# Kernel tuning notes

Measured on AMD Instinct MI355X. Metric: run time of the kernel, lower is better.

Reference implementation:

```python
import jax, jax.numpy as jnp
import numpy as np

P = 7            # cfg.PATCH_SIZE_PHOTOMETRIC
BRIGHT = 0.02    # bright_threshold
BIG = 1e9        # masks invalid points out of kNN
K = 5            # neighbors for smoothness/slope


def _smooth_l1(x, y, beta):
    d = jnp.abs(x - y)
    return jnp.where(d < beta, 0.5 * d * d / beta, d - 0.5 * beta)


def _sample_patches(img, kp):
    # img: [B,1,H,W], kp: [B,N,2] (x,y) in pixel coords -> [B,1,N,P,P]
    # matches F.grid_sample(align_corners=True, bilinear, border): with the
    # module's normalization, sampling positions are exactly pixel coords.
    B, _, H, W = img.shape
    N = kp.shape[1]
    half = P // 2
    lin = jnp.linspace(-half, half, P)
    oy, ox = jnp.meshgrid(lin, lin, indexing='ij')  # patch index (i,j): +x=lin[j], +y=lin[i]
    px = jnp.clip(kp[..., 0:1] + ox.ravel(), 0.0, W - 1)  # [B,N,P*P]
    py = jnp.clip(kp[..., 1:2] + oy.ravel(), 0.0, H - 1)
    x0 = jnp.floor(px); y0 = jnp.floor(py)
    fx = px - x0; fy = py - y0
    x0i = jnp.clip(x0.astype(jnp.int32), 0, W - 1)
    x1i = jnp.clip(x0i + 1, 0, W - 1)
    y0i = jnp.clip(y0.astype(jnp.int32), 0, H - 1)
    y1i = jnp.clip(y0i + 1, 0, H - 1)
    im = img[:, 0]  # [B,H,W]
    b = jnp.arange(B)[:, None, None]
    v00 = im[b, y0i, x0i]; v01 = im[b, y0i, x1i]
    v10 = im[b, y1i, x0i]; v11 = im[b, y1i, x1i]
    val = (v00 * (1 - fx) + v01 * fx) * (1 - fy) + (v10 * (1 - fx) + v11 * fx) * fy
    return val.reshape(B, 1, N, P, P)


def _forward(lg, rg, kpl, kpr, scores, Q):
    B, N, _ = kpl.shape
    # ---- epipolar ----
    y_diff = jnp.abs(kpl[..., 1] - kpr[..., 1])
    ws = scores.sum()
    l_epipolar = jnp.where(ws > 1e-4, (y_diff * scores).sum() / jnp.maximum(ws, 1e-12), y_diff.mean())
    # ---- photometric + intensity ----
    pl = _sample_patches(lg, kpl)
    pr = _sample_patches(rg, kpr)
    c = P // 2
    center_l = pl[:, 0, :, c, c]  # [B,N]
    center_r = pr[:, 0, :, c, c]
    is_bright = (center_l > BRIGHT).astype(pl.dtype)
    diff = jnp.abs(pl - pr).mean(axis=(1, 3, 4))  # [B,N]
    w = scores * is_bright
    wsum = w.sum()
    safe = jnp.maximum(wsum, 1e-12)
    l_masked = jnp.where(wsum > 1e-4, (diff * w).sum() / safe, 0.0)
    l_intensity = jnp.where(wsum > 1e-4, (_smooth_l1(center_l, center_r, 1.0) * w).sum() / safe, 0.0)
    l_photo = l_masked + l_intensity
    # ---- disparity -> 3D ----
    disp = kpl[..., 0] - kpr[..., 0]
    pts4 = jnp.concatenate([kpl, disp[..., None], jnp.ones((B, N, 1), kpl.dtype)], axis=-1)
    proj = jnp.einsum('bni,bji->bnj', pts4, Q)
    Wc = jnp.maximum(proj[..., 3], 1e-6)
    p3d = proj[..., :3] / Wc[..., None]  # [B,N,3]
    Z = p3d[..., 2]
    valid = (Z > 100) & (Z < 30000) & (scores > 0.1)  # [B,N]
    # ---- kNN smoothness / slope / zero-mean (masked, vectorized) ----
    pm = p3d / 1000.0
    xy = pm[..., jnp.array([0, 2])]  # [B,N,2] horizontal plane
    h = pm[..., 1]                   # [B,N] height
    sq = (xy * xy).sum(-1)
    d2 = sq[:, :, None] + sq[:, None, :] - 2.0 * jnp.einsum('bnd,bmd->bnm', xy, xy)
    dist = jnp.sqrt(jnp.maximum(d2, 1e-12))  # [B,N,N]
    vm = valid[:, :, None] & valid[:, None, :]
    dist = jnp.where(vm, dist, BIG)
    negd, idx = jax.lax.top_k(-dist, K + 1)   # ascending distance
    nbr_idx = idx[:, :, 1:]                   # drop self
    nbr_d = jnp.maximum(-negd[:, :, 1:], 1e-3)
    b = jnp.arange(B)[:, None, None]
    nbr_h = h[b, nbr_idx]                     # [B,N,K]
    local_mean = nbr_h.mean(-1)
    n_valid = valid.sum(-1)
    nv = jnp.maximum(n_valid, 1).astype(h.dtype)
    vf = valid.astype(h.dtype)
    ls_b = (_smooth_l1(h, local_mean, 0.01) * vf).sum(-1) / nv
    slopes = jnp.abs(nbr_h - h[..., None]) / nbr_d
    pen = jax.nn.relu(slopes - 0.4)
    lsl_b = (pen * vf[..., None]).sum((-1, -2)) / (nv * K)
    lz_b = jnp.abs((h * vf).sum(-1) / nv)
    ok = (n_valid >= 10).astype(h.dtype)
    nb = jnp.maximum(ok.sum(), 1.0)
    gate = ((scores > 0.1).sum() >= 10) & (ok.sum() > 0)
    l_smooth = jnp.where(gate, (ls_b * ok).sum() / nb, 0.0)
    l_slope = jnp.where(gate, (lsl_b * ok).sum() / nb, 0.0)
    l_zeromean = jnp.where(gate, (lz_b * ok).sum() / nb, 0.0)
    return (l_photo, l_epipolar, l_smooth, l_slope, l_zeromean)


def setup_inputs() -> dict:
    key = jax.random.key(0)
    k = jax.random.split(key, 7)
    B, N, H, W = 16, 2000, 720, 1280
    lg = jax.random.uniform(k[0], (B, 1, H, W), dtype=jnp.float32)
    rg = jax.random.uniform(k[1], (B, 1, H, W), dtype=jnp.float32)
    kx = jax.random.uniform(k[2], (B, N), minval=200.0, maxval=1080.0)
    ky = jax.random.uniform(k[3], (B, N), minval=50.0, maxval=670.0)
    disp = jax.random.uniform(k[4], (B, N), minval=10.0, maxval=200.0)
    kpl = jnp.stack([kx, ky], -1)
    kpr = jnp.stack([kx - disp, ky + 0.5 * jax.random.normal(k[5], (B, N))], -1)
    scores = jax.random.uniform(k[6], (B, N), dtype=jnp.float32)
    f, cx, cy, Tx = 1000.0, 640.0, 360.0, 120.0  # focal px, principal point, baseline mm
    Qm = jnp.array([[1.0, 0.0, 0.0, -cx],
                    [0.0, 1.0, 0.0, -cy],
                    [0.0, 0.0, 0.0, f],
                    [0.0, 0.0, 1.0 / Tx, 0.0]], dtype=jnp.float32)
    Q = jnp.broadcast_to(Qm, (B, 4, 4))
    return {"lg": lg, "rg": rg, "kpl": kpl, "kpr": kpr, "scores": scores, "Q": Q}


def reference(lg, rg, kpl, kpr, scores, Q):
    return _forward(lg, rg, kpl, kpr, scores, Q)
```

## Files before the change

### kernel.cpp

```cpp
#include <hip/hip_runtime.h>

#define BB 16
#define NN 2000
#define HH 720
#define WW 1280
#define NPT (BB*NN)
#define PATCH_BLOCKS (NPT/32)
#define PROJ_BLOCKS (NPT/256)
#define KSTRIDE 2048
#define MAX_SEG 500

static __device__ __forceinline__ unsigned u_min(unsigned a, unsigned b){ return a < b ? a : b; }

static __device__ __forceinline__ unsigned u_med3(unsigned a, unsigned b, unsigned c) {
    unsigned d;
    asm("v_med3_u32 %0, %1, %2, %3" : "=v"(d) : "v"(a), "v"(b), "v"(c));
    return d;
}

__device__ __forceinline__ void ins5(unsigned K[5], unsigned u) {
    K[4] = u_med3(K[3], K[4], u);
    K[3] = u_med3(K[2], K[3], u);
    K[2] = u_med3(K[1], K[2], u);
    K[1] = u_med3(K[0], K[1], u);
    K[0] = u_min(K[0], u);
}

__device__ __forceinline__ float bilin(const float* __restrict__ im, float px, float py) {
    px = fminf(fmaxf(px, 0.f), (float)(WW - 1));
    py = fminf(fmaxf(py, 0.f), (float)(HH - 1));
    float x0f = floorf(px), y0f = floorf(py);
    float fx = px - x0f, fy = py - y0f;
    int x0 = min(max((int)x0f, 0), WW - 1);
    int x1 = min(x0 + 1, WW - 1);
    int y0 = min(max((int)y0f, 0), HH - 1);
    int y1 = min(y0 + 1, HH - 1);
    const float* r0 = im + (size_t)y0 * WW;
    const float* r1 = im + (size_t)y1 * WW;
    float v00 = r0[x0], v01 = r0[x1], v10 = r1[x0], v11 = r1[x1];
    return (v00 * (1.f - fx) + v01 * fx) * (1.f - fy)
         + (v10 * (1.f - fx) + v11 * fx) * fy;
}

__global__ __launch_bounds__(256) void project_kernel(
    const float* __restrict__ kpl, const float* __restrict__ kpr,
    const float* __restrict__ scores, const float* __restrict__ Q,
    float4* __restrict__ pts, float* __restrict__ partialsA,
    float* __restrict__ batch_acc, unsigned* __restrict__ dcnt)
{
    if (blockIdx.x == 0) {
        if (threadIdx.x < BB * 4) batch_acc[threadIdx.x] = 0.f;
        if (threadIdx.x == BB * 4) *dcnt = 0u;
    }
    int pt = blockIdx.x * 256 + threadIdx.x;
    int b  = pt / NN;

    float2 kl = ((const float2* __restrict__)kpl)[pt];
    float2 kr = ((const float2* __restrict__)kpr)[pt];
    float sc  = scores[pt];
    float ydiff = fabsf(kl.y - kr.y);

    const float* q = Q + b * 16;
    float dsp = kl.x - kr.x;
    float p0 = q[0]*kl.x  + q[1]*kl.y  + q[2]*dsp  + q[3];
    float p1 = q[4]*kl.x  + q[5]*kl.y  + q[6]*dsp  + q[7];
    float p2 = q[8]*kl.x  + q[9]*kl.y  + q[10]*dsp + q[11];
    float p3 = q[12]*kl.x + q[13]*kl.y + q[14]*dsp + q[15];
    float Wc = fmaxf(p3, 1e-6f);
    float X = p0 / Wc, Y = p1 / Wc, Z = p2 / Wc;
    bool valid = (Z > 100.f) && (Z < 30000.f) && (sc > 0.1f);
    float x  = X / 1000.f;
    float hh = Y / 1000.f;
    float y  = Z / 1000.f;
    float sq = x * x + y * y;
    if (!valid) { x = 0.f; y = 0.f; sq = 1e18f; }
    pts[pt] = make_float4(x, y, sq, hh);

    float s0 = sc, s1 = ydiff * sc, s2 = ydiff, s3 = (sc > 0.1f) ? 1.f : 0.f;
    #pragma unroll
    for (int off = 32; off > 0; off >>= 1) {
        s0 += __shfl_down(s0, off, 64);
        s1 += __shfl_down(s1, off, 64);
        s2 += __shfl_down(s2, off, 64);
        s3 += __shfl_down(s3, off, 64);
    }
    __shared__ float red[4][4];
    int wave = threadIdx.x >> 6, lane = threadIdx.x & 63;
    if (lane == 0) { red[wave][0]=s0; red[wave][1]=s1; red[wave][2]=s2; red[wave][3]=s3; }
    __syncthreads();
    if (threadIdx.x < 4) {
        int k = threadIdx.x;
        partialsA[blockIdx.x * 4 + k] = red[0][k] + red[1][k] + red[2][k] + red[3][k];
    }
}

__global__ __launch_bounds__(256) void fused_patch_scan(
    const float* __restrict__ lg, const float* __restrict__ rg,
    const float* __restrict__ kpl, const float* __restrict__ kpr,
    const float* __restrict__ scores,
    const float4* __restrict__ pts, unsigned* __restrict__ keybuf,
    float* __restrict__ partialsB, int msegLen, int lns, int interleave)
{
    int i = blockIdx.x;
    int pid, sid;
    if (interleave) {
        if ((i % 3 == 1) && (i < 3000)) { pid = i / 3;  sid = -1; }
        else { pid = -1; sid = i - ((i < 3000) ? (i + 2) / 3 : 1000); }
    } else {
        if (i < PATCH_BLOCKS) { pid = i; sid = -1; }
        else { pid = -1; sid = i - PATCH_BLOCKS; }
    }

    if (pid >= 0) {
        int wave = threadIdx.x >> 6, lane = threadIdx.x & 63;
        int rr = lane / 7, ci = lane - rr * 7;
        int s00 = lane + rr;
        if (s00 > 54) s00 = 54;
        int reg_r = lane >> 3, reg_c = lane & 7;

        float a3 = 0.f, a4l = 0.f, a5 = 0.f;

        for (int it = 0; it < 8; ++it) {
            int pt = pid * 32 + wave * 8 + it;
            int b = pt / NN;
            const float* iml = lg + (size_t)b * (HH * WW);
            const float* imr = rg + (size_t)b * (HH * WW);
            float kxl = kpl[2*pt], kyl = kpl[2*pt+1];
            float kxr = kpr[2*pt], kyr = kpr[2*pt+1];
            float sc  = scores[pt];

            float flx = floorf(kxl), fly = floorf(kyl);
            int xbl = (int)flx - 3, ybl = (int)fly - 3;
            float fxl = kxl - flx, fyl = kyl - fly;
            float vl = 0.f;
            if (xbl >= 0 && xbl <= WW-8 && ybl >= 0 && ybl <= HH-8) {
                float reg = iml[(size_t)(ybl + reg_r) * WW + xbl + reg_c];
                float v00 = __shfl(reg, s00,     64);
                float v01 = __shfl(reg, s00 + 1, 64);
                float v10 = __shfl(reg, s00 + 8, 64);
                float v11 = __shfl(reg, s00 + 9, 64);
                vl = (v00*(1.f-fxl) + v01*fxl)*(1.f-fyl) + (v10*(1.f-fxl) + v11*fxl)*fyl;
            } else if (lane < 49) {
                vl = bilin(iml, kxl + (float)(ci-3), kyl + (float)(rr-3));
            }
            float frx = floorf(kxr), fry = floorf(kyr);
            int xbr = (int)frx - 3, ybr = (int)fry - 3;
            float fxr = kxr - frx, fyr = kyr - fry;
            float vr = 0.f;
            if (xbr >= 0 && xbr <= WW-8 && ybr >= 0 && ybr <= HH-8) {
                float reg = imr[(size_t)(ybr + reg_r) * WW + xbr + reg_c];
                float v00 = __shfl(reg, s00,     64);
                float v01 = __shfl(reg, s00 + 1, 64);
                float v10 = __shfl(reg, s00 + 8, 64);
                float v11 = __shfl(reg, s00 + 9, 64);
                vr = (v00*(1.f-fxr) + v01*fxr)*(1.f-fyr) + (v10*(1.f-fxr) + v11*fxr)*fyr;
            } else if (lane < 49) {
                vr = bilin(imr, kxr + (float)(ci-3), kyr + (float)(rr-3));
            }

            float adiff = (lane < 49) ? fabsf(vl - vr) : 0.f;
            float cl = __shfl(vl, 24, 64);
            float cr = __shfl(vr, 24, 64);

            float isb = (cl > 0.02f) ? 1.f : 0.f;
            float w   = sc * isb;
            float dc  = fabsf(cl - cr);
            float sl1 = (dc < 1.f) ? 0.5f * dc * dc : dc - 0.5f;

            a3 += w;
            a5 += sl1 * w;
            a4l += w * adiff;
        }

        #pragma unroll
        for (int off = 32; off > 0; off >>= 1) a4l += __shfl_down(a4l, off, 64);

        __shared__ float red[4][3];
        if (lane == 0) { red[wave][0]=a3; red[wave][1]=a4l * (1.f/49.f); red[wave][2]=a5; }
        __syncthreads();
        if (threadIdx.x < 4) {
            int k = threadIdx.x;
            float v = 0.f;
            if (k < 3) v = red[0][k] + red[1][k] + red[2][k] + red[3][k];
            partialsB[pid * 4 + k] = v;
        }
    } else {
        __shared__ float4 seg[MAX_SEG];
        int sblk = sid;
        int bx   = sblk & 7;
        int r    = sblk >> 3;
        int segi = r & ((1 << lns) - 1);
        int b    = r >> lns;
        int ns   = 1 << lns;
        int mseg0 = segi * msegLen;
        int n = bx * 256 + threadIdx.x;
        int nc = (n < NN) ? n : (NN - 1);

        const float4* cand = pts + b * NN + mseg0;
        for (int j = threadIdx.x; j < msegLen; j += 256) seg[j] = cand[j];

        float4 me = pts[b * NN + nc];
        float nx2 = -2.f * me.x, ny2 = -2.f * me.y, sqn = me.z;

        unsigned K[5] = {0xFFFFFFFFu,0xFFFFFFFFu,0xFFFFFFFFu,0xFFFFFFFFu,0xFFFFFFFFu};

        int nb0 = bx * 256;
        bool has_self = (mseg0 < nb0 + 256) && (mseg0 + msegLen > nb0);

        __syncthreads();

        if (has_self) {
            #pragma unroll 5
            for (int mm = 0; mm < msegLen; ++mm) {
                float4 o = seg[mm];
                int m = mseg0 + mm;
                float t = fmaf(ny2, o.y, o.z);
                t = fmaf(nx2, o.x, t);
                float d2 = fmaxf(t + sqn, 1e-12f);
                unsigned u = (__float_as_uint(d2) & 0xFFFFF800u) | (unsigned)m;
                u = (m == n) ? 0xFFFFFFFFu : u;
                ins5(K, u);
            }
        } else {
            #pragma unroll 5
            for (int mm = 0; mm < msegLen; ++mm) {
                float4 o = seg[mm];
                int m = mseg0 + mm;
                float t = fmaf(ny2, o.y, o.z);
                t = fmaf(nx2, o.x, t);
                float d2 = fmaxf(t + sqn, 1e-12f);
                unsigned u = (__float_as_uint(d2) & 0xFFFFF800u) | (unsigned)m;
                ins5(K, u);
            }
        }

        if (n < NN) {
            size_t base = (size_t)((b * ns + segi) * 5) * KSTRIDE + n;
            keybuf[base              ] = K[0];
            keybuf[base + KSTRIDE    ] = K[1];
            keybuf[base + KSTRIDE * 2] = K[2];
            keybuf[base + KSTRIDE * 3] = K[3];
            keybuf[base + KSTRIDE * 4] = K[4];
        }
    }
}

__global__ __launch_bounds__(256) void knn_merge_final(
    const float4* __restrict__ pts, const unsigned* __restrict__ keybuf,
    float* __restrict__ batch_acc, unsigned* __restrict__ dcnt,
    const float* __restrict__ partialsA, const float* __restrict__ partialsB,
    float* __restrict__ out, int ns)
{
    int b = blockIdx.y;
    int n = blockIdx.x * 256 + threadIdx.x;

    float ls = 0.f, pen = 0.f, hacc = 0.f, cnt = 0.f;
    if (n < NN) {
        float4 me = pts[b * NN + n];
        if (me.z < 1e17f) {
            unsigned K[5] = {0xFFFFFFFFu,0xFFFFFFFFu,0xFFFFFFFFu,0xFFFFFFFFu,0xFFFFFFFFu};
            for (int s = 0; s < ns; ++s) {
                #pragma unroll
                for (int j = 0; j < 5; ++j) {
                    unsigned u = keybuf[(size_t)((b * ns + s) * 5 + j) * KSTRIDE + n];
                    ins5(K, u);
                }
            }
            float hsum = 0.f;
            #pragma unroll
            for (int t = 0; t < 5; ++t) {
                int idx = (int)(K[t] & 2047u);
                float4 o = pts[b * NN + idx];
                float dot = me.x * o.x + me.y * o.y;
                float d2 = (me.z + o.z) - 2.f * dot;
                float nd = fmaxf(sqrtf(fmaxf(d2, 1e-12f)), 0.001f);
                hsum += o.w;
                pen  += fmaxf(fabsf(o.w - me.w) / nd - 0.4f, 0.f);
            }
            float lm = hsum / 5.f;
            float dd = fabsf(me.w - lm);
            ls = (dd < 0.01f) ? 0.5f * dd * dd / 0.01f : dd - 0.005f;
            hacc = me.w;
            cnt  = 1.f;
        }
    }

    #pragma unroll
    for (int off = 32; off > 0; off >>= 1) {
        ls   += __shfl_down(ls,   off, 64);
        pen  += __shfl_down(pen,  off, 64);
        hacc += __shfl_down(hacc, off, 64);
        cnt  += __shfl_down(cnt,  off, 64);
    }
    __shared__ float r2[4][4];
    int wave = threadIdx.x >> 6, lane = threadIdx.x & 63;
    if (lane == 0) { r2[wave][0]=cnt; r2[wave][1]=ls; r2[wave][2]=pen; r2[wave][3]=hacc; }
    __syncthreads();
    if (threadIdx.x == 0) {
        float tc = r2[0][0]+r2[1][0]+r2[2][0]+r2[3][0];
        float tl = r2[0][1]+r2[1][1]+r2[2][1]+r2[3][1];
        float tp = r2[0][2]+r2[1][2]+r2[2][2]+r2[3][2];
        float th = r2[0][3]+r2[1][3]+r2[2][3]+r2[3][3];
        atomicAdd(&batch_acc[b * 4 + 0], tc);
        atomicAdd(&batch_acc[b * 4 + 1], tl);
        atomicAdd(&batch_acc[b * 4 + 2], tp);
        atomicAdd(&batch_acc[b * 4 + 3], th);
    }

    __shared__ int lastf;
    __threadfence();
    if (threadIdx.x == 0) {
        unsigned old = atomicAdd(dcnt, 1u);
        lastf = (old == (unsigned)(8 * BB - 1)) ? 1 : 0;
    }
    __syncthreads();
    if (!lastf) return;
    __threadfence();

    float s[7] = {0,0,0,0,0,0,0};
    for (int rI = threadIdx.x; rI < PROJ_BLOCKS; rI += 256) {
        s[0] += partialsA[rI * 4 + 0];
        s[1] += partialsA[rI * 4 + 1];
        s[2] += partialsA[rI * 4 + 2];
        s[3] += partialsA[rI * 4 + 3];
    }
    for (int rI = threadIdx.x; rI < PATCH_BLOCKS; rI += 256) {
        s[4] += partialsB[rI * 4 + 0];
        s[5] += partialsB[rI * 4 + 1];
        s[6] += partialsB[rI * 4 + 2];
    }
    #pragma unroll
    for (int off = 32; off > 0; off >>= 1) {
        #pragma unroll
        for (int k = 0; k < 7; ++k) s[k] += __shfl_down(s[k], off, 64);
    }
    __shared__ float ws2[4][7];
    if (lane == 0) {
        #pragma unroll
        for (int k = 0; k < 7; ++k) ws2[wave][k] = s[k];
    }
    __syncthreads();
    if (threadIdx.x == 0) {
        float t[7];
        #pragma unroll
        for (int k = 0; k < 7; ++k)
            t[k] = ws2[0][k] + ws2[1][k] + ws2[2][k] + ws2[3][k];
        float ssc = t[0], yds = t[1], yd = t[2], cnts = t[3];
        float wsum = t[4], dw = t[5], iw = t[6];

        float l_epi = (ssc > 1e-4f) ? yds / fmaxf(ssc, 1e-12f) : yd / (float)NPT;
        float safe = fmaxf(wsum, 1e-12f);
        float l_photo = (wsum > 1e-4f) ? (dw / safe + iw / safe) : 0.f;

        float als = 0.f, alsl = 0.f, alz = 0.f, okc = 0.f;
        for (int bb = 0; bb < BB; ++bb) {
            float nvf  = __hip_atomic_load(&batch_acc[bb*4+0], __ATOMIC_RELAXED, __HIP_MEMORY_SCOPE_AGENT);
            float lsb  = __hip_atomic_load(&batch_acc[bb*4+1], __ATOMIC_RELAXED, __HIP_MEMORY_SCOPE_AGENT);
            float penb = __hip_atomic_load(&batch_acc[bb*4+2], __ATOMIC_RELAXED, __HIP_MEMORY_SCOPE_AGENT);
            float hb   = __hip_atomic_load(&batch_acc[bb*4+3], __ATOMIC_RELAXED, __HIP_MEMORY_SCOPE_AGENT);
            float nv = fmaxf(nvf, 1.f);
            float ok = (nvf >= 10.f) ? 1.f : 0.f;
            als  += ok * (lsb / nv);
            alsl += ok * (penb / (nv * 5.f));
            alz  += ok * fabsf(hb / nv);
            okc  += ok;
        }
        float nb = fmaxf(okc, 1.f);
        bool gate = (cnts >= 10.f) && (okc > 0.f);
        out[0] = l_photo;
        out[1] = l_epi;
        out[2] = gate ? als / nb : 0.f;
        out[3] = gate ? alsl / nb : 0.f;
        out[4] = gate ? alz / nb : 0.f;
    }
}

extern "C" void kernel_launch(void* const* d_in, const int* in_sizes, int n_in,
                              void* d_out, int out_size, void* d_ws, size_t ws_size,
                              hipStream_t stream)
{
    const float* lg     = (const float*)d_in[0];
    const float* rg     = (const float*)d_in[1];
    const float* kpl    = (const float*)d_in[2];
    const float* kpr    = (const float*)d_in[3];
    const float* scores = (const float*)d_in[4];
    const float* Q      = (const float*)d_in[5];
    float* out = (float*)d_out;

    char* ws = (char*)d_ws;
    float4*   pts       = (float4*)ws;
    float*    partialsA = (float*)(ws + 512000);
    float*    partialsB = (float*)(ws + 514048);
    float*    batch_acc = (float*)(ws + 530432);
    unsigned* dcnt      = (unsigned*)(ws + 530688);
    unsigned* keybuf    = (unsigned*)(ws + 530944);

    int ns = 16;
    if (ws_size < 530944 + (size_t)BB * 16 * 5 * KSTRIDE * 4) ns = 8;
    if (ws_size < 530944 + (size_t)BB *  8 * 5 * KSTRIDE * 4) ns = 4;
    int lns = (ns == 16) ? 4 : ((ns == 8) ? 3 : 2);
    int msegLen = NN / ns;
    int interleave = (ns == 16) ? 1 : 0;

    project_kernel<<<PROJ_BLOCKS, 256, 0, stream>>>(kpl, kpr, scores, Q,
                                                    pts, partialsA, batch_acc, dcnt);
    fused_patch_scan<<<PATCH_BLOCKS + 8 * ns * BB, 256, 0, stream>>>(
        lg, rg, kpl, kpr, scores, pts, keybuf, partialsB, msegLen, lns, interleave);
    knn_merge_final<<<dim3(8, BB), 256, 0, stream>>>(pts, keybuf, batch_acc, dcnt,
                                                     partialsA, partialsB, out, ns);
}
```

Measured before the change: 178.7 us.

## Split patch work to one point per wave and interleave 4:1 with scan blocks

The patch-sampling part of the fused kernel now gives each wave a single keypoint instead of looping over eight, so there are 8000 patch blocks instead of 1000. Patch blocks are interleaved four to one with kNN scan blocks, and the left and right image loads are issued together before the shuffles. The goal is more memory-level parallelism and better load balance between the two block types. The cost is more blocks, a larger partials buffer (workspace offsets shift) and a longer final reduction over 8000 partials.

```diff
diff --git a/kernel.cpp b/kernel.cpp
--- a/kernel.cpp
+++ b/kernel.cpp
@@ -5,7 +5,7 @@
 #define HH 720
 #define WW 1280
 #define NPT (BB*NN)
-#define PATCH_BLOCKS (NPT/32)
+#define PB_BLOCKS (NPT/4)
 #define PROJ_BLOCKS (NPT/256)
 #define KSTRIDE 2048
 #define MAX_SEG 500
@@ -104,79 +104,78 @@
     int i = blockIdx.x;
     int pid, sid;
     if (interleave) {
-        if ((i % 3 == 1) && (i < 3000)) { pid = i / 3;  sid = -1; }
-        else { pid = -1; sid = i - ((i < 3000) ? (i + 2) / 3 : 1000); }
+        if ((i % 5) == 0) { sid = i / 5; pid = -1; }
+        else { pid = (i / 5) * 4 + (i % 5) - 1; sid = -1; }
     } else {
-        if (i < PATCH_BLOCKS) { pid = i; sid = -1; }
-        else { pid = -1; sid = i - PATCH_BLOCKS; }
+        if (i < PB_BLOCKS) { pid = i; sid = -1; }
+        else { pid = -1; sid = i - PB_BLOCKS; }
     }
 
     if (pid >= 0) {
+        if (pid >= PB_BLOCKS) return;
         int wave = threadIdx.x >> 6, lane = threadIdx.x & 63;
         int rr = lane / 7, ci = lane - rr * 7;
         int s00 = lane + rr;
         if (s00 > 54) s00 = 54;
         int reg_r = lane >> 3, reg_c = lane & 7;
 
-        float a3 = 0.f, a4l = 0.f, a5 = 0.f;
-
-        for (int it = 0; it < 8; ++it) {
-            int pt = pid * 32 + wave * 8 + it;
-            int b = pt / NN;
-            const float* iml = lg + (size_t)b * (HH * WW);
-            const float* imr = rg + (size_t)b * (HH * WW);
-            float kxl = kpl[2*pt], kyl = kpl[2*pt+1];
-            float kxr = kpr[2*pt], kyr = kpr[2*pt+1];
-            float sc  = scores[pt];
-
-            float flx = floorf(kxl), fly = floorf(kyl);
-            int xbl = (int)flx - 3, ybl = (int)fly - 3;
-            float fxl = kxl - flx, fyl = kyl - fly;
-            float vl = 0.f;
-            if (xbl >= 0 && xbl <= WW-8 && ybl >= 0 && ybl <= HH-8) {
-                float reg = iml[(size_t)(ybl + reg_r) * WW + xbl + reg_c];
-                float v00 = __shfl(reg, s00,     64);
-                float v01 = __shfl(reg, s00 + 1, 64);
-                float v10 = __shfl(reg, s00 + 8, 64);
-                float v11 = __shfl(reg, s00 + 9, 64);
-                vl = (v00*(1.f-fxl) + v01*fxl)*(1.f-fyl) + (v10*(1.f-fxl) + v11*fxl)*fyl;
-            } else if (lane < 49) {
-                vl = bilin(iml, kxl + (float)(ci-3), kyl + (float)(rr-3));
-            }
-            float frx = floorf(kxr), fry = floorf(kyr);
-            int xbr = (int)frx - 3, ybr = (int)fry - 3;
-            float fxr = kxr - frx, fyr = kyr - fry;
-            float vr = 0.f;
-            if (xbr >= 0 && xbr <= WW-8 && ybr >= 0 && ybr <= HH-8) {
-                float reg = imr[(size_t)(ybr + reg_r) * WW + xbr + reg_c];
-                float v00 = __shfl(reg, s00,     64);
-                float v01 = __shfl(reg, s00 + 1, 64);
-                float v10 = __shfl(reg, s00 + 8, 64);
-                float v11 = __shfl(reg, s00 + 9, 64);
-                vr = (v00*(1.f-fxr) + v01*fxr)*(1.f-fyr) + (v10*(1.f-fxr) + v11*fxr)*fyr;
-            } else if (lane < 49) {
-                vr = bilin(imr, kxr + (float)(ci-3), kyr + (float)(rr-3));
-            }
-
-            float adiff = (lane < 49) ? fabsf(vl - vr) : 0.f;
-            float cl = __shfl(vl, 24, 64);
-            float cr = __shfl(vr, 24, 64);
-
+        int pt = pid * 4 + wave;
+        int b = pt / NN;
+        const float* iml = lg + (size_t)b * (HH * WW);
+        const float* imr = rg + (size_t)b * (HH * WW);
+        float kxl = kpl[2*pt], kyl = kpl[2*pt+1];
+        float kxr = kpr[2*pt], kyr = kpr[2*pt+1];
+        float sc  = scores[pt];
+
+        float flx = floorf(kxl), fly = floorf(kyl);
+        float frx = floorf(kxr), fry = floorf(kyr);
+        int xbl = (int)flx - 3, ybl = (int)fly - 3;
+        int xbr = (int)frx - 3, ybr = (int)fry - 3;
+        float fxl = kxl - flx, fyl = kyl - fly;
+        float fxr = kxr - frx, fyr = kyr - fry;
+        bool inL = (xbl >= 0) && (xbl <= WW-8) && (ybl >= 0) && (ybl <= HH-8);
+        bool inR = (xbr >= 0) && (xbr <= WW-8) && (ybr >= 0) && (ybr <= HH-8);
+
+        float regL = 0.f, regR = 0.f;
+        if (inL) regL = iml[(size_t)(ybl + reg_r) * WW + xbl + reg_c];
+        if (inR) regR = imr[(size_t)(ybr + reg_r) * WW + xbr + reg_c];
+
+        float vl = 0.f, vr = 0.f;
+        if (inL) {
+            float v00 = __shfl(regL, s00,     64);
+            float v01 = __shfl(regL, s00 + 1, 64);
+            float v10 = __shfl(regL, s00 + 8, 64);
+            float v11 = __shfl(regL, s00 + 9, 64);
+            vl = (v00*(1.f-fxl) + v01*fxl)*(1.f-fyl) + (v10*(1.f-fxl) + v11*fxl)*fyl;
+        } else if (lane < 49) {
+            vl = bilin(iml, kxl + (float)(ci-3), kyl + (float)(rr-3));
+        }
+        if (inR) {
+            float v00 = __shfl(regR, s00,     64);
+            float v01 = __shfl(regR, s00 + 1, 64);
+            float v10 = __shfl(regR, s00 + 8, 64);
+            float v11 = __shfl(regR, s00 + 9, 64);
+            vr = (v00*(1.f-fxr) + v01*fxr)*(1.f-fyr) + (v10*(1.f-fxr) + v11*fxr)*fyr;
+        } else if (lane < 49) {
+            vr = bilin(imr, kxr + (float)(ci-3), kyr + (float)(rr-3));
+        }
+
+        float adiff = (lane < 49) ? fabsf(vl - vr) : 0.f;
+        float cl = __shfl(vl, 24, 64);
+        float cr = __shfl(vr, 24, 64);
+        #pragma unroll
+        for (int off = 32; off > 0; off >>= 1) adiff += __shfl_down(adiff, off, 64);
+
+        __shared__ float red[4][3];
+        if (lane == 0) {
             float isb = (cl > 0.02f) ? 1.f : 0.f;
             float w   = sc * isb;
             float dc  = fabsf(cl - cr);
             float sl1 = (dc < 1.f) ? 0.5f * dc * dc : dc - 0.5f;
-
-            a3 += w;
-            a5 += sl1 * w;
-            a4l += w * adiff;
-        }
-
-        #pragma unroll
-        for (int off = 32; off > 0; off >>= 1) a4l += __shfl_down(a4l, off, 64);
-
-        __shared__ float red[4][3];
-        if (lane == 0) { red[wave][0]=a3; red[wave][1]=a4l * (1.f/49.f); red[wave][2]=a5; }
+            red[wave][0] = w;
+            red[wave][1] = w * adiff * (1.f/49.f);
+            red[wave][2] = sl1 * w;
+        }
         __syncthreads();
         if (threadIdx.x < 4) {
             int k = threadIdx.x;
@@ -324,7 +323,7 @@
         s[2] += partialsA[rI * 4 + 2];
         s[3] += partialsA[rI * 4 + 3];
     }
-    for (int rI = threadIdx.x; rI < PATCH_BLOCKS; rI += 256) {
+    for (int rI = threadIdx.x; rI < PB_BLOCKS; rI += 256) {
         s[4] += partialsB[rI * 4 + 0];
         s[5] += partialsB[rI * 4 + 1];
         s[6] += partialsB[rI * 4 + 2];
@@ -391,20 +390,22 @@
     float4*   pts       = (float4*)ws;
     float*    partialsA = (float*)(ws + 512000);
     float*    partialsB = (float*)(ws + 514048);
-    float*    batch_acc = (float*)(ws + 530432);
-    unsigned* dcnt      = (unsigned*)(ws + 530688);
-    unsigned* keybuf    = (unsigned*)(ws + 530944);
+    float*    batch_acc = (float*)(ws + 645120);
+    unsigned* dcnt      = (unsigned*)(ws + 645376);
+    unsigned* keybuf    = (unsigned*)(ws + 645632);
 
     int ns = 16;
-    if (ws_size < 530944 + (size_t)BB * 16 * 5 * KSTRIDE * 4) ns = 8;
-    if (ws_size < 530944 + (size_t)BB *  8 * 5 * KSTRIDE * 4) ns = 4;
+    if (ws_size < 645632 + (size_t)BB * 16 * 5 * KSTRIDE * 4) ns = 8;
+    if (ws_size < 645632 + (size_t)BB *  8 * 5 * KSTRIDE * 4) ns = 4;
     int lns = (ns == 16) ? 4 : ((ns == 8) ? 3 : 2);
     int msegLen = NN / ns;
     int interleave = (ns == 16) ? 1 : 0;
 
+    int nblk = interleave ? 10240 : (PB_BLOCKS + 8 * ns * BB);
+
     project_kernel<<<PROJ_BLOCKS, 256, 0, stream>>>(kpl, kpr, scores, Q,
                                                     pts, partialsA, batch_acc, dcnt);
-    fused_patch_scan<<<PATCH_BLOCKS + 8 * ns * BB, 256, 0, stream>>>(
+    fused_patch_scan<<<nblk, 256, 0, stream>>>(
         lg, rg, kpl, kpr, scores, pts, keybuf, partialsB, msegLen, lns, interleave);
     knn_merge_final<<<dim3(8, BB), 256, 0, stream>>>(pts, keybuf, batch_acc, dcnt,
                                                      partialsA, partialsB, out, ns);
```

After: 188.4 us. +5.4%, slower.
